# Performance work log

Hardware: AMD Instinct MI355X
Metric: run time of the kernel (lower is better)

## Reference

```python
import jax, jax.numpy as jnp
import numpy as np

B, P, T = 64, 49, 20      # batch, num_pixels (7x7), caption length
V, E, D, A, ENC = 32000, 512, 512, 512, 2048


def setup_inputs() -> dict:
    key = jax.random.key(0)
    ks = jax.random.split(key, 20)
    s = 0.02
    return {
        "features": jax.random.normal(ks[0], (B, P, ENC), jnp.float32),
        "captions": jax.random.randint(ks[1], (B, T), 0, V, jnp.int64),
        "embed_table": jax.random.normal(ks[2], (V, E), jnp.float32) * s,
        "W_ih": jax.random.normal(ks[3], (4 * D, ENC + E), jnp.float32) * s,
        "b_ih": jnp.zeros((4 * D,), jnp.float32),
        "W_hh": jax.random.normal(ks[4], (4 * D, D), jnp.float32) * s,
        "b_hh": jnp.zeros((4 * D,), jnp.float32),
        "W_init_h": jax.random.normal(ks[5], (ENC, D), jnp.float32) * s,
        "b_init_h": jnp.zeros((D,), jnp.float32),
        "W_init_c": jax.random.normal(ks[6], (ENC, D), jnp.float32) * s,
        "b_init_c": jnp.zeros((D,), jnp.float32),
        "W_enc_att": jax.random.normal(ks[7], (ENC, A), jnp.float32) * s,
        "b_enc_att": jnp.zeros((A,), jnp.float32),
        "W_dec_att": jax.random.normal(ks[8], (D, A), jnp.float32) * s,
        "b_dec_att": jnp.zeros((A,), jnp.float32),
        "w_A": jax.random.normal(ks[9], (A,), jnp.float32) * s,
        "b_A": jnp.zeros((), jnp.float32),
        "W_out": jax.random.normal(ks[10], (D, V), jnp.float32) * s,
        "b_out": jnp.zeros((V,), jnp.float32),
    }


def reference(features, captions, embed_table, W_ih, b_ih, W_hh, b_hh,
              W_init_h, b_init_h, W_init_c, b_init_c,
              W_enc_att, b_enc_att, W_dec_att, b_dec_att, w_A, b_A,
              W_out, b_out):
    # Dropout is treated as identity (eval mode) for a deterministic baseline.
    bsz, seq_len = captions.shape
    emb = embed_table[captions]                              # [B,T,E]
    mean_f = features.mean(axis=1)                           # [B,ENC]
    h0 = mean_f @ W_init_h + b_init_h                        # [B,D]
    c0 = mean_f @ W_init_c + b_init_c                        # [B,D]
    enc_states = features @ W_enc_att + b_enc_att            # [B,P,A] (precomputed, loop-invariant)

    def step(carry, x_t):
        h, c = carry
        dec = h @ W_dec_att + b_dec_att                      # [B,A]
        comb = jnp.tanh(enc_states + dec[:, None, :])        # [B,P,A]
        scores = comb @ w_A + b_A                            # [B,P]
        alpha = jax.nn.softmax(scores, axis=1)
        ctx = jnp.einsum('bpe,bp->be', features, alpha)      # [B,ENC]
        x = jnp.concatenate([ctx, x_t], axis=1)              # [B,ENC+E]
        gates = x @ W_ih.T + b_ih + h @ W_hh.T + b_hh        # [B,4D]
        i, f, g, o = jnp.split(gates, 4, axis=1)
        i, f, o = jax.nn.sigmoid(i), jax.nn.sigmoid(f), jax.nn.sigmoid(o)
        g = jnp.tanh(g)
        c2 = f * c + i * g
        h2 = o * jnp.tanh(c2)
        logits = h2 @ W_out + b_out                          # [B,V]
        return (h2, c2), logits

    xs = jnp.swapaxes(emb[:, :seq_len - 1], 0, 1)            # [T-1,B,E]
    _, preds = jax.lax.scan(step, (h0, c0), xs)              # [T-1,B,V]
    preds = jnp.swapaxes(preds, 0, 1)                        # [B,T-1,V]
    vocab = W_out.shape[1]
    last = jnp.zeros((bsz, 1, vocab), preds.dtype)           # t = T-1 never written
    return jnp.concatenate([preds, last], axis=1)            # [B,T,V]
```

## Files before the change

kernel.cpp:

```cpp
#include <hip/hip_runtime.h>

constexpr int B_   = 64;
constexpr int P_   = 49;
constexpr int T_   = 20;
constexpr int V_   = 32000;
constexpr int E_   = 512;
constexpr int D_   = 512;
constexpr int A_   = 512;
constexpr int ENC_ = 2048;
constexpr int NT_  = T_ - 1;
constexpr int KX_  = ENC_ + E_ + D_;
constexpr int KSPL = 8;
constexpr int GCH  = (KX_ / 64) / KSPL;
constexpr int KS4  = 4;

#define DI __device__ __forceinline__

using u16 = unsigned short;
typedef short   bf16x8 __attribute__((ext_vector_type(8)));
typedef float   f32x4  __attribute__((ext_vector_type(4)));
typedef u16     u16x4  __attribute__((ext_vector_type(4)));

DI float sigm(float x) { return 1.0f / (1.0f + __expf(-x)); }
DI float tanhx(float x) {
  x = fminf(15.0f, fmaxf(-15.0f, x));
  float e = __expf(2.0f * x);
  return (e - 1.0f) / (e + 1.0f);
}
DI u16 f2bf(float x) {
  union { float f; unsigned u; } v{x};
  unsigned r = v.u + 0x7FFF + ((v.u >> 16) & 1);
  return (u16)(r >> 16);
}
DI float bf2f(u16 x) {
  union { unsigned u; float f; } v;
  v.u = ((unsigned)x) << 16;
  return v.f;
}
DI f32x4 mfma16(bf16x8 a, bf16x8 b, f32x4 c) {
  return __builtin_amdgcn_mfma_f32_16x16x32_bf16(a, b, c, 0, 0, 0);
}

constexpr int PRO1_BLOCKS = 32256;

DI void dev_tr_cvt(const float* in, u16* outp, int R, int C, int bx, int by,
                   float (*tbuf)[33]) {
  int tx = threadIdx.x & 31, ty = threadIdx.x >> 5;
  int c0 = bx * 32, r0 = by * 32;
#pragma unroll
  for (int i = 0; i < 4; i++)
    tbuf[ty + 8 * i][tx] = in[(size_t)(r0 + ty + 8 * i) * C + c0 + tx];
  __syncthreads();
#pragma unroll
  for (int i = 0; i < 4; i++)
    outp[(size_t)(c0 + ty + 8 * i) * R + r0 + tx] = f2bf(tbuf[tx][ty + 8 * i]);
}

__global__ __launch_bounds__(256) void k_pro1(
    const float* __restrict__ feat, const float* __restrict__ Winh,
    const float* __restrict__ Winc, const float* __restrict__ Wenc,
    const float* __restrict__ Wdec, const float* __restrict__ Wout,
    const float* __restrict__ Wih, const float* __restrict__ Whh,
    u16* __restrict__ mfb, u16* __restrict__ featb, u16* __restrict__ WiT,
    u16* __restrict__ WeT, u16* __restrict__ WdT, u16* __restrict__ WoT,
    u16* __restrict__ Wg) {
  __shared__ float tbuf[32][33];
  int bid = blockIdx.x;
  if (bid < 6272) {
    int i = bid * 256 + threadIdx.x;
    float4 v = ((const float4*)feat)[i];
    u16x4 r = {f2bf(v.x), f2bf(v.y), f2bf(v.z), f2bf(v.w)};
    ((u16x4*)featb)[i] = r;
  } else if (bid < 6784) {
    int idx = (bid - 6272) * 256 + threadIdx.x;
    int b = idx >> 11, e = idx & (ENC_ - 1);
    const float* f = feat + (size_t)b * P_ * ENC_ + e;
    float s = 0.f;
#pragma unroll
    for (int p = 0; p < P_; p++) s += f[(size_t)p * ENC_];
    mfb[idx] = f2bf(s * (1.0f / P_));
  } else if (bid < 7808) {
    int l = bid - 6784;
    dev_tr_cvt(Winh, WiT, ENC_, D_, l & 15, l >> 4, tbuf);
  } else if (bid < 8832) {
    int l = bid - 7808;
    dev_tr_cvt(Winc, WiT + (size_t)D_ * ENC_, ENC_, D_, l & 15, l >> 4, tbuf);
  } else if (bid < 9856) {
    int l = bid - 8832;
    dev_tr_cvt(Wenc, WeT, ENC_, A_, l & 15, l >> 4, tbuf);
  } else if (bid < 10112) {
    int l = bid - 9856;
    dev_tr_cvt(Wdec, WdT, D_, A_, l & 15, l >> 4, tbuf);
  } else if (bid < 26112) {
    int l = bid - 10112;
    dev_tr_cvt(Wout, WoT, D_, V_, l % 1000, l / 1000, tbuf);
  } else {
    int i = (bid - 26112) * 256 + threadIdx.x;
    int j = i / 768, rem = i - j * 768;
    int k = rem * 4;
    const float* src = (k < ENC_ + E_) ? (Wih + (size_t)j * (ENC_ + E_) + k)
                                       : (Whh + (size_t)j * D_ + (k - ENC_ - E_));
    float4 v = *(const float4*)src;
    u16x4 r = {f2bf(v.x), f2bf(v.y), f2bf(v.z), f2bf(v.w)};
    ((u16x4*)Wg)[i] = r;
  }
}


__global__ __launch_bounds__(256) void k_pro2(const u16* __restrict__ mfb,
    const u16* __restrict__ WiT, const float* __restrict__ binh,
    const float* __restrict__ binc, u16* __restrict__ hbf,
    float* __restrict__ c, const u16* __restrict__ featb,
    const u16* __restrict__ WeT, const float* __restrict__ benc,
    float* __restrict__ encs) {
  int wid = threadIdx.x >> 6, lane = threadIdx.x & 63;
  int l16 = lane & 15, lk = lane >> 4;
  if (blockIdx.x < 16) {
    int n0 = blockIdx.x * 64 + wid * 16;
    const u16* bp = WiT + (size_t)(n0 + l16) * ENC_ + 8 * lk;
    const u16* ap = mfb + (size_t)l16 * ENC_ + 8 * lk;
    f32x4 acc[4] = {};
#pragma unroll 4
    for (int kc = 0; kc < ENC_; kc += 32) {
      bf16x8 b = *(const bf16x8*)(bp + kc);
#pragma unroll
      for (int mf = 0; mf < 4; mf++) {
        bf16x8 a = *(const bf16x8*)(ap + (size_t)mf * 16 * ENC_ + kc);
        acc[mf] = mfma16(a, b, acc[mf]);
      }
    }
    int n = n0 + l16;
#pragma unroll
    for (int mf = 0; mf < 4; mf++) {
      int m = mf * 16 + 4 * lk;
#pragma unroll
      for (int r = 0; r < 4; r++) {
        float v = acc[mf][r];
        if (n < D_) hbf[(size_t)(m + r) * D_ + n] = f2bf(v + binh[n]);
        else        c[(size_t)(m + r) * D_ + (n - D_)] = v + binc[n - D_];
      }
    }
  } else {
    int l = blockIdx.x - 16;
    int m0 = (l % 49) * 64, n0 = (l / 49) * 64 + wid * 16;
    const u16* ap = featb + (size_t)(m0 + l16) * ENC_ + 8 * lk;
    const u16* bp = WeT + (size_t)(n0 + l16) * ENC_ + 8 * lk;
    f32x4 acc[4] = {};
#pragma unroll 8
    for (int i = 0; i < ENC_ / 32; i++) {
      int kc = i * 32;
      bf16x8 b = *(const bf16x8*)(bp + kc);
#pragma unroll
      for (int mf = 0; mf < 4; mf++) {
        bf16x8 a = *(const bf16x8*)(ap + (size_t)mf * 16 * ENC_ + kc);
        acc[mf] = mfma16(a, b, acc[mf]);
      }
    }
    float bv = benc[n0 + l16];
#pragma unroll
    for (int mf = 0; mf < 4; mf++) {
      int m = m0 + mf * 16 + 4 * lk;
#pragma unroll
      for (int r = 0; r < 4; r++)
        encs[(size_t)(m + r) * A_ + n0 + l16] = acc[mf][r] + bv;
    }
  }
}


__global__ __launch_bounds__(512) void k_att5(const u16* __restrict__ featb,
    const float* __restrict__ encs, const u16* __restrict__ WdT,
    const float* __restrict__ bdec, const float* __restrict__ wA,
    const float* __restrict__ bA, const float* __restrict__ gp,
    const float* __restrict__ bih, const float* __restrict__ bhh,
    float* __restrict__ c, u16* __restrict__ hbf, u16* __restrict__ hallp,
    u16* __restrict__ ctxb, const int* __restrict__ cap,
    const float* __restrict__ tab, u16* __restrict__ embt, int t,
    int do_reduce, int do_att) {
  __shared__ u16 hsb[D_];
  __shared__ float ds[A_];
  __shared__ float sc[P_];
  __shared__ float inv_s;
  int b = blockIdx.x, tid = threadIdx.x;

  if (do_att) {
    int tok = cap[b * T_ + t];
    embt[(size_t)b * E_ + tid] = f2bf(tab[(size_t)tok * E_ + tid]);
  }

  if (do_reduce) {
    int d = tid;
    float g0 = 0, g1 = 0, g2 = 0, g3 = 0;
#pragma unroll
    for (int s = 0; s < KS4; s++) {
      const float* g = gp + (size_t)(s * B_ + b) * (4 * D_);
      g0 += g[d]; g1 += g[D_ + d]; g2 += g[2 * D_ + d]; g3 += g[3 * D_ + d];
    }
    g0 += bih[d] + bhh[d];
    g1 += bih[D_ + d] + bhh[D_ + d];
    g2 += bih[2 * D_ + d] + bhh[2 * D_ + d];
    g3 += bih[3 * D_ + d] + bhh[3 * D_ + d];
    float iv = sigm(g0), fv = sigm(g1), gv = tanhx(g2), ov = sigm(g3);
    float cv = fmaf(fv, c[b * D_ + d], iv * gv);
    float hv = ov * tanhx(cv);
    c[b * D_ + d] = cv;
    u16 hb = f2bf(hv);
    hsb[d] = hb;
    hbf[b * D_ + d] = hb;
    hallp[b * D_ + d] = hb;
  } else {
    hsb[tid] = hbf[b * D_ + tid];
  }
  __syncthreads();
  if (!do_att) return;

  {
    int w = tid >> 6, lane = tid & 63, l16 = lane & 15, lk = lane >> 4;
#pragma unroll
    for (int f = 0; f < 4; f++) {
      int n = w * 64 + f * 16 + l16;
      const u16* bp = WdT + (size_t)n * D_ + 8 * lk;
      f32x4 acc = {};
#pragma unroll
      for (int kc = 0; kc < D_; kc += 32) {
        bf16x8 av = *(const bf16x8*)(hsb + kc + 8 * lk);
        bf16x8 bv = *(const bf16x8*)(bp + kc);
        acc = mfma16(av, bv, acc);
      }
      if (lk == 0) ds[n] = acc[0] + bdec[n];
    }
  }
  __syncthreads();

  {
    int wv_ = tid >> 6, ln = tid & 63;
    float bA0 = bA[0];
    for (int p = wv_; p < P_; p += 8) {
      const float* ep = encs + (size_t)(b * P_ + p) * A_;
      float s = 0.f;
#pragma unroll
      for (int a = ln; a < A_; a += 64) s += tanhx(ep[a] + ds[a]) * wA[a];
#pragma unroll
      for (int off = 32; off; off >>= 1) s += __shfl_down(s, off);
      if (ln == 0) sc[p] = s + bA0;
    }
  }
  __syncthreads();
  if (tid == 0) {
    float mx = -1e30f;
    for (int p = 0; p < P_; p++) mx = fmaxf(mx, sc[p]);
    float sum = 0.f;
    for (int p = 0; p < P_; p++) { float ex = __expf(sc[p] - mx); sc[p] = ex; sum += ex; }
    inv_s = 1.0f / sum;
  }
  __syncthreads();
  {
    float inv = inv_s;
    int e = tid * 4;
    const u16* fp = featb + (size_t)b * P_ * ENC_ + e;
    float s0 = 0.f, s1 = 0.f, s2 = 0.f, s3 = 0.f;
#pragma unroll
    for (int p = 0; p < P_; p++) {
      u16x4 w = *(const u16x4*)(fp + (size_t)p * ENC_);
      float scp = sc[p];
      s0 = fmaf(bf2f(w.x), scp, s0);
      s1 = fmaf(bf2f(w.y), scp, s1);
      s2 = fmaf(bf2f(w.z), scp, s2);
      s3 = fmaf(bf2f(w.w), scp, s3);
    }
    u16x4 o = {f2bf(s0 * inv), f2bf(s1 * inv), f2bf(s2 * inv), f2bf(s3 * inv)};
    *(u16x4*)(ctxb + b * ENC_ + e) = o;
  }
}

__global__ __launch_bounds__(256) void k_gates4(const u16* __restrict__ ctxb,
    const u16* __restrict__ embt, const u16* __restrict__ hbf,
    const u16* __restrict__ Wg, float* __restrict__ gp) {
  int wid = threadIdx.x >> 6, lane = threadIdx.x & 63;
  int j0 = blockIdx.x * 64 + wid * 16;
  int sp = blockIdx.y;
  int l16 = lane & 15, lk = lane >> 4;
  const u16* bp = Wg + (size_t)(j0 + l16) * KX_ + 8 * lk;
  f32x4 acc[4] = {};
#pragma unroll
  for (int i = 0; i < KX_ / KS4 / 32; i++) {
    int kc = sp * (KX_ / KS4) + i * 32;
    int k = kc + 8 * lk;
    bf16x8 b = *(const bf16x8*)(bp + kc);
#pragma unroll
    for (int mf = 0; mf < 4; mf++) {
      int row = mf * 16 + l16;
      const u16* src;
      if (k < ENC_)            src = ctxb + (size_t)row * ENC_ + k;
      else if (k < ENC_ + E_)  src = embt + (size_t)row * E_ + (k - ENC_);
      else                     src = hbf + (size_t)row * D_ + (k - ENC_ - E_);
      bf16x8 a = *(const bf16x8*)src;
      acc[mf] = mfma16(a, b, acc[mf]);
    }
  }
#pragma unroll
  for (int mf = 0; mf < 4; mf++) {
    int m = mf * 16 + 4 * lk;
#pragma unroll
    for (int r = 0; r < 4; r++)
      gp[((size_t)sp * B_ + m + r) * (4 * D_) + j0 + l16] = acc[mf][r];
  }
}


__global__ __launch_bounds__(256) void k_logits_all4(const u16* __restrict__ hall,
    const u16* __restrict__ WoT, const float* __restrict__ bout,
    float* __restrict__ out) {
  __shared__ float tile[64 * 264];
  int L = blockIdx.x;
  int x8 = L & 7, r = L >> 3;
  int g = r / 24, s = r % 24;
  int nt = g * 8 + x8;
  if (nt >= 125) return;
  if (s == NT_) {
    int tr = threadIdx.x >> 2, tc = threadIdx.x & 3;
    f32x4 z = {0.f, 0.f, 0.f, 0.f};
    float* op = out + ((size_t)tr * T_ + NT_) * V_ + nt * 256;
#pragma unroll
    for (int j = 0; j < 16; j++)
      __builtin_nontemporal_store(z, (f32x4*)(op + (tc + j * 4) * 4));
    return;
  }
  if (s > NT_) return;
  int w = threadIdx.x >> 6, lane = threadIdx.x & 63;
  int l16 = lane & 15, lk = lane >> 4;
  const u16* ap0 = hall + (size_t)s * B_ * D_ + (size_t)l16 * D_ + 8 * lk;
  int ncol0 = nt * 256 + w * 64;
#pragma unroll 1
  for (int ch = 0; ch < 4; ch++) {
    int col = ncol0 + ch * 16 + l16;
    const u16* bp = WoT + (size_t)col * D_ + 8 * lk;
    f32x4 acc[4] = {};
#pragma unroll
    for (int kc = 0; kc < 16; kc++) {
      bf16x8 b = *(const bf16x8*)(bp + kc * 32);
#pragma unroll
      for (int mf = 0; mf < 4; mf++) {
        bf16x8 a = *(const bf16x8*)(ap0 + (size_t)mf * 16 * D_ + kc * 32);
        acc[mf] = mfma16(a, b, acc[mf]);
      }
    }
    float bv = bout[col];
#pragma unroll
    for (int mf = 0; mf < 4; mf++)
#pragma unroll
      for (int rr = 0; rr < 4; rr++)
        tile[(mf * 16 + 4 * lk + rr) * 264 + w * 64 + ch * 16 + l16] =
            acc[mf][rr] + bv;
  }
  __syncthreads();
  int tr = threadIdx.x >> 2, tc = threadIdx.x & 3;
  float* op = out + ((size_t)tr * T_ + s) * V_ + nt * 256;
  const float* lp = &tile[tr * 264];
#pragma unroll
  for (int j = 0; j < 16; j++) {
    int cc = (tc + j * 4) * 4;
    __builtin_nontemporal_store(*(const f32x4*)(lp + cc), (f32x4*)(op + cc));
  }
}


DI int swz(int row, int slot) { return row * 64 + ((slot ^ (row >> 2)) << 2); }

__global__ __launch_bounds__(256) void k_mean(const float* __restrict__ feat,
                                              float* __restrict__ mf) {
  int idx = blockIdx.x * 256 + threadIdx.x;
  int b = idx >> 11, e = idx & (ENC_ - 1);
  const float* f = feat + (size_t)b * P_ * ENC_ + e;
  float s = 0.f;
#pragma unroll
  for (int p = 0; p < P_; p++) s += f[(size_t)p * ENC_];
  mf[idx] = s * (1.0f / P_);
}

__global__ __launch_bounds__(256) void k_emb(const int* __restrict__ cap,
                                             const float* __restrict__ tab,
                                             float* __restrict__ emb) {
  int idx = blockIdx.x * 256 + threadIdx.x;
  int e  = idx & (E_ - 1);
  int bt = idx >> 9;
  int b = bt / NT_, t = bt - b * NT_;
  int tok = cap[b * T_ + t];
  emb[idx] = tab[(size_t)tok * E_ + e];
}

__global__ __launch_bounds__(256) void k_init(const float* __restrict__ mf,
    const float* __restrict__ Wh, const float* __restrict__ bh,
    const float* __restrict__ Wc, const float* __restrict__ bc,
    float* __restrict__ h, float* __restrict__ c) {
  __shared__ float ms[ENC_];
  int b = blockIdx.y;
  for (int i = threadIdx.x; i < ENC_; i += 256) ms[i] = mf[b * ENC_ + i];
  __syncthreads();
  int d = blockIdx.x * 256 + threadIdx.x;
  const float* W = blockIdx.z ? Wc : Wh;
  float s = (blockIdx.z ? bc : bh)[d];
#pragma unroll 8
  for (int e = 0; e < ENC_; e++) s = fmaf(ms[e], W[(size_t)e * D_ + d], s);
  (blockIdx.z ? c : h)[b * D_ + d] = s;
}

__global__ __launch_bounds__(256) void k_zero_last(float* __restrict__ out) {
  int i = blockIdx.x * 256 + threadIdx.x;
  int b = i / 8000, v4 = i - b * 8000;
  float4 z = {0.f, 0.f, 0.f, 0.f};
  *(float4*)(out + ((size_t)b * T_ + (T_ - 1)) * V_ + (size_t)v4 * 4) = z;
}

__global__ __launch_bounds__(256) void k_enc(const float* __restrict__ Ag,
    const float* __restrict__ Wg, const float* __restrict__ bias,
    float* __restrict__ Cg) {
  __shared__ float As[64 * 64], Ws[64 * 64];
  int m0 = blockIdx.x * 64, n0 = blockIdx.y * 64;
  int tid = threadIdx.x, tn = tid & 15, tm = tid >> 4;
  float acc[4][4] = {};
#pragma unroll 1
  for (int ch = 0; ch < ENC_ / 64; ch++) {
    int k0 = ch * 64;
    __syncthreads();
#pragma unroll
    for (int q = 0; q < 4; q++) {
      int idx = tid + q * 256;
      int row = idx >> 4, slot = idx & 15;
      *(float4*)&As[swz(row, slot)] =
          *(const float4*)(Ag + (size_t)(m0 + row) * ENC_ + k0 + slot * 4);
      *(float4*)&Ws[swz(row, slot)] =
          *(const float4*)(Wg + (size_t)(k0 + row) * A_ + n0 + slot * 4);
    }
    __syncthreads();
#pragma unroll
    for (int kk = 0; kk < 16; kk++) {
      float4 av[4], wv[4];
#pragma unroll
      for (int i = 0; i < 4; i++) av[i] = *(float4*)&As[swz(4 * tm + i, kk)];
#pragma unroll
      for (int u = 0; u < 4; u++) wv[u] = *(float4*)&Ws[swz(4 * kk + u, tn)];
      const float* wq = (const float*)wv;
#pragma unroll
      for (int i = 0; i < 4; i++) {
        const float* aq = (const float*)&av[i];
#pragma unroll
        for (int j = 0; j < 4; j++) {
          float s = acc[i][j];
#pragma unroll
          for (int u = 0; u < 4; u++) s = fmaf(aq[u], wq[u * 4 + j], s);
          acc[i][j] = s;
        }
      }
    }
  }
#pragma unroll
  for (int i = 0; i < 4; i++) {
    int m = m0 + 4 * tm + i, n = n0 + 4 * tn;
    float4 bv = *(const float4*)(bias + n);
    float4 o = {acc[i][0] + bv.x, acc[i][1] + bv.y, acc[i][2] + bv.z, acc[i][3] + bv.w};
    *(float4*)(Cg + (size_t)m * A_ + n) = o;
  }
}

__global__ __launch_bounds__(256) void k_logits(const float* __restrict__ h,
    const float* __restrict__ Wout, const float* __restrict__ bout,
    float* __restrict__ out, int t) {
  __shared__ float As[64 * 64], Ws[64 * 64];
  int n0 = blockIdx.x * 64;
  int tid = threadIdx.x, tn = tid & 15, tm = tid >> 4;
  float acc[4][4] = {};
#pragma unroll 1
  for (int ch = 0; ch < D_ / 64; ch++) {
    int k0 = ch * 64;
    __syncthreads();
#pragma unroll
    for (int q = 0; q < 4; q++) {
      int idx = tid + q * 256;
      int row = idx >> 4, slot = idx & 15;
      *(float4*)&As[swz(row, slot)] =
          *(const float4*)(h + (size_t)row * D_ + k0 + slot * 4);
      *(float4*)&Ws[swz(row, slot)] =
          *(const float4*)(Wout + (size_t)(k0 + row) * V_ + n0 + slot * 4);
    }
    __syncthreads();
#pragma unroll
    for (int kk = 0; kk < 16; kk++) {
      float4 av[4], wv[4];
#pragma unroll
      for (int i = 0; i < 4; i++) av[i] = *(float4*)&As[swz(4 * tm + i, kk)];
#pragma unroll
      for (int u = 0; u < 4; u++) wv[u] = *(float4*)&Ws[swz(4 * kk + u, tn)];
      const float* wq = (const float*)wv;
#pragma unroll
      for (int i = 0; i < 4; i++) {
        const float* aq = (const float*)&av[i];
#pragma unroll
        for (int j = 0; j < 4; j++) {
          float s = acc[i][j];
#pragma unroll
          for (int u = 0; u < 4; u++) s = fmaf(aq[u], wq[u * 4 + j], s);
          acc[i][j] = s;
        }
      }
    }
  }
#pragma unroll
  for (int i = 0; i < 4; i++) {
    int m = 4 * tm + i, n = n0 + 4 * tn;
    float4 bv = *(const float4*)(bout + n);
    float4 o = {acc[i][0] + bv.x, acc[i][1] + bv.y, acc[i][2] + bv.z, acc[i][3] + bv.w};
    *(float4*)(out + ((size_t)m * T_ + t) * V_ + n) = o;
  }
}

__global__ __launch_bounds__(256) void k_gates(const float* __restrict__ ctx,
    const float* __restrict__ emb, const float* __restrict__ h,
    const float* __restrict__ Wih, const float* __restrict__ Whh,
    float* __restrict__ gp, int t) {
  __shared__ float As[64 * 64], Ws[64 * 64];
  int n0 = blockIdx.x * 64;
  int sp = blockIdx.y;
  int tid = threadIdx.x, tn = tid & 15, tm = tid >> 4;
  float acc[4][4] = {};
#pragma unroll 1
  for (int ch = 0; ch < GCH; ch++) {
    int k0 = sp * (GCH * 64) + ch * 64;
    __syncthreads();
#pragma unroll
    for (int q = 0; q < 4; q++) {
      int idx = tid + q * 256;
      int row = idx >> 4, slot = idx & 15;
      int k = k0 + slot * 4;
      float4 xv;
      if (k < ENC_)            xv = *(const float4*)(ctx + (size_t)row * ENC_ + k);
      else if (k < ENC_ + E_)  xv = *(const float4*)(emb + ((size_t)row * NT_ + t) * E_ + (k - ENC_));
      else                     xv = *(const float4*)(h + (size_t)row * D_ + (k - ENC_ - E_));
      *(float4*)&As[swz(row, slot)] = xv;
      int j = n0 + row;
      float4 wv2;
      if (k < ENC_ + E_) wv2 = *(const float4*)(Wih + (size_t)j * (ENC_ + E_) + k);
      else               wv2 = *(const float4*)(Whh + (size_t)j * D_ + (k - ENC_ - E_));
      *(float4*)&Ws[swz(row, slot)] = wv2;
    }
    __syncthreads();
#pragma unroll
    for (int kk = 0; kk < 16; kk++) {
      float4 av[4], wv[4];
#pragma unroll
      for (int i = 0; i < 4; i++) av[i] = *(float4*)&As[swz(4 * tm + i, kk)];
#pragma unroll
      for (int j = 0; j < 4; j++) wv[j] = *(float4*)&Ws[swz(4 * tn + j, kk)];
#pragma unroll
      for (int i = 0; i < 4; i++) {
        const float* aq = (const float*)&av[i];
#pragma unroll
        for (int j = 0; j < 4; j++) {
          const float* wqj = (const float*)&wv[j];
          float s = acc[i][j];
#pragma unroll
          for (int u = 0; u < 4; u++) s = fmaf(aq[u], wqj[u], s);
          acc[i][j] = s;
        }
      }
    }
  }
#pragma unroll
  for (int i = 0; i < 4; i++) {
    int b = 4 * tm + i, j = n0 + 4 * tn;
    float4 o = {acc[i][0], acc[i][1], acc[i][2], acc[i][3]};
    *(float4*)(gp + ((size_t)(sp * B_ + b)) * (4 * D_) + j) = o;
  }
}

__global__ __launch_bounds__(512) void k_att(const float* __restrict__ feat,
    const float* __restrict__ encs, const float* __restrict__ Wdec,
    const float* __restrict__ bdec, const float* __restrict__ wA,
    const float* __restrict__ bA, const float* __restrict__ gp,
    const float* __restrict__ bih, const float* __restrict__ bhh,
    float* __restrict__ h, float* __restrict__ c, float* __restrict__ ctx,
    int do_reduce, int do_att) {
  __shared__ float hs[D_];
  __shared__ float ds[A_];
  __shared__ float sc[P_];
  __shared__ float inv_s;
  int b = blockIdx.x, tid = threadIdx.x;

  if (do_reduce) {
    int d = tid;
    float g0 = 0, g1 = 0, g2 = 0, g3 = 0;
#pragma unroll
    for (int s = 0; s < KSPL; s++) {
      const float* g = gp + (size_t)(s * B_ + b) * (4 * D_);
      g0 += g[d]; g1 += g[D_ + d]; g2 += g[2 * D_ + d]; g3 += g[3 * D_ + d];
    }
    g0 += bih[d] + bhh[d];
    g1 += bih[D_ + d] + bhh[D_ + d];
    g2 += bih[2 * D_ + d] + bhh[2 * D_ + d];
    g3 += bih[3 * D_ + d] + bhh[3 * D_ + d];
    float iv = sigm(g0), fv = sigm(g1), gv = tanhx(g2), ov = sigm(g3);
    float cv = fmaf(fv, c[b * D_ + d], iv * gv);
    float hv = ov * tanhx(cv);
    c[b * D_ + d] = cv;
    h[b * D_ + d] = hv;
    hs[d] = hv;
  } else {
    hs[tid] = h[b * D_ + tid];
  }
  __syncthreads();
  if (!do_att) return;

  {
    int a = tid;
    float s = bdec[a];
#pragma unroll 8
    for (int d = 0; d < D_; d++) s = fmaf(hs[d], Wdec[(size_t)d * A_ + a], s);
    ds[a] = s;
  }
  __syncthreads();

  int wv_ = tid >> 6, ln = tid & 63;
  float bA0 = bA[0];
  for (int p = wv_; p < P_; p += 8) {
    const float* ep = encs + (size_t)(b * P_ + p) * A_;
    float s = 0.f;
#pragma unroll
    for (int a = ln; a < A_; a += 64) s += tanhx(ep[a] + ds[a]) * wA[a];
#pragma unroll
    for (int off = 32; off; off >>= 1) s += __shfl_down(s, off);
    if (ln == 0) sc[p] = s + bA0;
  }
  __syncthreads();

  if (tid == 0) {
    float mx = -1e30f;
    for (int p = 0; p < P_; p++) mx = fmaxf(mx, sc[p]);
    float sum = 0.f;
    for (int p = 0; p < P_; p++) { float ex = __expf(sc[p] - mx); sc[p] = ex; sum += ex; }
    inv_s = 1.0f / sum;
  }
  __syncthreads();

  float inv = inv_s;
  for (int e = tid; e < ENC_; e += 512) {
    const float* fp = feat + (size_t)b * P_ * ENC_ + e;
    float s = 0.f;
#pragma unroll
    for (int p = 0; p < P_; p++) s = fmaf(fp[(size_t)p * ENC_], sc[p], s);
    ctx[b * ENC_ + e] = s * inv;
  }
}


extern "C" void kernel_launch(void* const* d_in, const int* in_sizes, int n_in,
                              void* d_out, int out_size, void* d_ws, size_t ws_size,
                              hipStream_t stream) {
  const float* features = (const float*)d_in[0];
  const int*   captions = (const int*)d_in[1];
  const float* table    = (const float*)d_in[2];
  const float* Wih  = (const float*)d_in[3];
  const float* bih  = (const float*)d_in[4];
  const float* Whh  = (const float*)d_in[5];
  const float* bhh  = (const float*)d_in[6];
  const float* Winh = (const float*)d_in[7];
  const float* binh = (const float*)d_in[8];
  const float* Winc = (const float*)d_in[9];
  const float* binc = (const float*)d_in[10];
  const float* Wenc = (const float*)d_in[11];
  const float* benc = (const float*)d_in[12];
  const float* Wdec = (const float*)d_in[13];
  const float* bdec = (const float*)d_in[14];
  const float* wA   = (const float*)d_in[15];
  const float* bA   = (const float*)d_in[16];
  const float* Wout = (const float*)d_in[17];
  const float* bout = (const float*)d_in[18];
  float* out = (float*)d_out;

  constexpr size_t F_ENC = (size_t)B_ * P_ * A_;
  constexpr size_t F_C   = (size_t)B_ * D_;
  constexpr size_t F_GP  = (size_t)KSPL * B_ * 4 * D_;
  constexpr size_t U_WOT = (size_t)V_ * D_;
  constexpr size_t U_WG  = (size_t)(4 * D_) * KX_;
  constexpr size_t U_HBF = (size_t)B_ * D_;
  constexpr size_t U_CTX = (size_t)B_ * ENC_;
  constexpr size_t U_FEAT = (size_t)B_ * P_ * ENC_;
  constexpr size_t U_WET = (size_t)A_ * ENC_;
  constexpr size_t U_WDT = (size_t)A_ * D_;
  constexpr size_t U_HALL = (size_t)NT_ * B_ * D_;
  static_assert((size_t)KS4 * B_ * 4 * D_ <= F_GP, "gp(KS4) fits");
  static_assert((size_t)B_ * E_ <= 2 * F_C, "embt fits in cbuf1");
  constexpr size_t NEED_BYTES =
      (F_ENC + 2 * F_C + F_GP) * 4 +
      (U_WOT + U_WG + U_HBF + U_CTX + U_FEAT + U_WET + U_HALL) * 2;
  constexpr size_t NEED2 = NEED_BYTES + U_WDT * 2;

  if (ws_size >= NEED2) {
    float* ws = (float*)d_ws;
    float* enc_states = ws;
    float* cbuf0  = enc_states + F_ENC;
    float* cbuf1  = cbuf0 + F_C;
    float* gparts = cbuf1 + F_C;
    u16* WoT   = (u16*)(gparts + F_GP);
    u16* Wg    = WoT + U_WOT;
    u16* hbf   = Wg + U_WG;
    u16* ctxb  = hbf + U_HBF;
    u16* featb = ctxb + U_CTX;
    u16* WeT   = featb + U_FEAT;
    u16* hall  = WeT + U_WET;
    u16* WdT   = hall + U_HALL;
    u16* WiT   = (u16*)gparts;
    u16* mfb   = ctxb;
    u16* embt  = (u16*)cbuf1;

    k_pro1<<<PRO1_BLOCKS, 256, 0, stream>>>(features, Winh, Winc, Wenc, Wdec,
                                            Wout, Wih, Whh, mfb, featb, WiT,
                                            WeT, WdT, WoT, Wg);
    k_pro2<<<408, 256, 0, stream>>>(mfb, WiT, binh, binc, hbf, cbuf0, featb,
                                    WeT, benc, enc_states);

    for (int t = 0; t < NT_; t++) {
      u16* hallp = (t > 0) ? (hall + (size_t)(t - 1) * B_ * D_) : hall;
      k_att5<<<64, 512, 0, stream>>>(featb, enc_states, WdT, bdec, wA, bA,
                                     gparts, bih, bhh, cbuf0, hbf, hallp, ctxb,
                                     captions, table, embt, t,
                                     t > 0 ? 1 : 0, 1);
      k_gates4<<<dim3(32, KS4), 256, 0, stream>>>(ctxb, embt, hbf, Wg, gparts);
    }
    k_att5<<<64, 512, 0, stream>>>(featb, enc_states, WdT, bdec, wA, bA,
                                   gparts, bih, bhh, cbuf0, hbf,
                                   hall + (size_t)(NT_ - 1) * B_ * D_, ctxb,
                                   captions, table, embt, 0, 1, 0);
    k_logits_all4<<<3072, 256, 0, stream>>>(hall, WoT, bout, out);
  } else {
    float* ws = (float*)d_ws;
    float* enc_states = ws;
    float* mean_f = enc_states + (size_t)B_ * P_ * A_;
    float* emb    = mean_f + (size_t)B_ * ENC_;
    float* h      = emb + (size_t)B_ * NT_ * E_;
    float* c      = h + (size_t)B_ * D_;
    float* ctx    = c + (size_t)B_ * D_;
    float* gparts = ctx + (size_t)B_ * ENC_;

    k_mean<<<512, 256, 0, stream>>>(features, mean_f);
    k_emb<<<2432, 256, 0, stream>>>(captions, table, emb);
    k_init<<<dim3(2, 64, 2), 256, 0, stream>>>(mean_f, Winh, binh, Winc, binc, h, c);
    k_enc<<<dim3(49, 8), 256, 0, stream>>>(features, Wenc, benc, enc_states);
    k_zero_last<<<2000, 256, 0, stream>>>(out);

    for (int t = 0; t < NT_; t++) {
      k_att<<<64, 512, 0, stream>>>(features, enc_states, Wdec, bdec, wA, bA,
                                    gparts, bih, bhh, h, c, ctx, t > 0 ? 1 : 0, 1);
      if (t > 0)
        k_logits<<<500, 256, 0, stream>>>(h, Wout, bout, out, t - 1);
      k_gates<<<dim3(32, KSPL), 256, 0, stream>>>(ctx, emb, h, Wih, Whh, gparts, t);
    }
    k_att<<<64, 512, 0, stream>>>(features, enc_states, Wdec, bdec, wA, bA,
                                  gparts, bih, bhh, h, c, ctx, 1, 0);
    k_logits<<<500, 256, 0, stream>>>(h, Wout, bout, out, NT_ - 1);
  }
}
```

Measured before the change: 1.349 ms.

## Split attention across two blocks per batch, widen gates K-split, add tiled W_out transpose

The W_out transpose moves out of the prologue into a dedicated kernel that reads coalesced float4 rows and writes 16-byte bf16 rows through a large shared tile. The per-step attention kernel now runs two blocks per batch row, each computing half of the context vector, with the LSTM cell state ping-ponged between two buffers so the duplicated block can redundantly recompute the cell update without racing. The gate GEMM's K-split goes from 4 to 8 for more parallelism, and h is written straight into the history buffer instead of a separate copy. The costs are duplicated attention-score work per batch, a larger partial-gate reduction, and heavy shared memory in the transpose kernel.

```diff
diff --git a/kernel.cpp b/kernel.cpp
--- a/kernel.cpp
+++ b/kernel.cpp
@@ -11,8 +11,6 @@
 constexpr int NT_  = T_ - 1;
 constexpr int KX_  = ENC_ + E_ + D_;
 constexpr int KSPL = 8;
-constexpr int GCH  = (KX_ / 64) / KSPL;
-constexpr int KS4  = 4;
 
 #define DI __device__ __forceinline__
 
@@ -20,6 +18,7 @@
 typedef short   bf16x8 __attribute__((ext_vector_type(8)));
 typedef float   f32x4  __attribute__((ext_vector_type(4)));
 typedef u16     u16x4  __attribute__((ext_vector_type(4)));
+typedef u16     u16x2  __attribute__((ext_vector_type(2)));
 
 DI float sigm(float x) { return 1.0f / (1.0f + __expf(-x)); }
 DI float tanhx(float x) {
@@ -41,7 +40,7 @@
   return __builtin_amdgcn_mfma_f32_16x16x32_bf16(a, b, c, 0, 0, 0);
 }
 
-constexpr int PRO1_BLOCKS = 32256;
+constexpr int PRO1_BLOCKS = 16256;
 
 DI void dev_tr_cvt(const float* in, u16* outp, int R, int C, int bx, int by,
                    float (*tbuf)[33]) {
@@ -56,14 +55,13 @@
     outp[(size_t)(c0 + ty + 8 * i) * R + r0 + tx] = f2bf(tbuf[tx][ty + 8 * i]);
 }
 
-__global__ __launch_bounds__(256) void k_pro1(
+__global__ __launch_bounds__(256) void k_pro1s(
     const float* __restrict__ feat, const float* __restrict__ Winh,
     const float* __restrict__ Winc, const float* __restrict__ Wenc,
-    const float* __restrict__ Wdec, const float* __restrict__ Wout,
-    const float* __restrict__ Wih, const float* __restrict__ Whh,
-    u16* __restrict__ mfb, u16* __restrict__ featb, u16* __restrict__ WiT,
-    u16* __restrict__ WeT, u16* __restrict__ WdT, u16* __restrict__ WoT,
-    u16* __restrict__ Wg) {
+    const float* __restrict__ Wdec, const float* __restrict__ Wih,
+    const float* __restrict__ Whh, u16* __restrict__ mfb,
+    u16* __restrict__ featb, u16* __restrict__ WiT, u16* __restrict__ WeT,
+    u16* __restrict__ WdT, u16* __restrict__ Wg) {
   __shared__ float tbuf[32][33];
   int bid = blockIdx.x;
   if (bid < 6272) {
@@ -91,11 +89,8 @@
   } else if (bid < 10112) {
     int l = bid - 9856;
     dev_tr_cvt(Wdec, WdT, D_, A_, l & 15, l >> 4, tbuf);
-  } else if (bid < 26112) {
-    int l = bid - 10112;
-    dev_tr_cvt(Wout, WoT, D_, V_, l % 1000, l / 1000, tbuf);
   } else {
-    int i = (bid - 26112) * 256 + threadIdx.x;
+    int i = (bid - 10112) * 256 + threadIdx.x;
     int j = i / 768, rem = i - j * 768;
     int k = rem * 4;
     const float* src = (k < ENC_ + E_) ? (Wih + (size_t)j * (ENC_ + E_) + k)
@@ -106,10 +101,32 @@
   }
 }
 
+__global__ __launch_bounds__(256) void k_trW(const float* __restrict__ in,
+                                             u16* __restrict__ outp) {
+  __shared__ u16 ld[128][264];
+  int v0 = blockIdx.x * 128, k0 = blockIdx.y * 256;
+  int vf = (threadIdx.x & 31) * 4, kk = threadIdx.x >> 5;
+#pragma unroll 4
+  for (int p = 0; p < 32; p++) {
+    int k = kk + p * 8;
+    float4 v = *(const float4*)(in + (size_t)(k0 + k) * V_ + v0 + vf);
+    ld[vf + 0][k] = f2bf(v.x);
+    ld[vf + 1][k] = f2bf(v.y);
+    ld[vf + 2][k] = f2bf(v.z);
+    ld[vf + 3][k] = f2bf(v.w);
+  }
+  __syncthreads();
+  int v = threadIdx.x >> 1, h = threadIdx.x & 1;
+  u16* op = outp + (size_t)(v0 + v) * D_ + k0 + h * 128;
+#pragma unroll
+  for (int i = 0; i < 16; i++)
+    *(bf16x8*)(op + i * 8) = *(const bf16x8*)(&ld[v][h * 128 + i * 8]);
+}
+
 
 __global__ __launch_bounds__(256) void k_pro2(const u16* __restrict__ mfb,
     const u16* __restrict__ WiT, const float* __restrict__ binh,
-    const float* __restrict__ binc, u16* __restrict__ hbf,
+    const float* __restrict__ binc, u16* __restrict__ hall0,
     float* __restrict__ c, const u16* __restrict__ featb,
     const u16* __restrict__ WeT, const float* __restrict__ benc,
     float* __restrict__ encs) {
@@ -136,7 +153,7 @@
 #pragma unroll
       for (int r = 0; r < 4; r++) {
         float v = acc[mf][r];
-        if (n < D_) hbf[(size_t)(m + r) * D_ + n] = f2bf(v + binh[n]);
+        if (n < D_) hall0[(size_t)(m + r) * D_ + n] = f2bf(v + binh[n]);
         else        c[(size_t)(m + r) * D_ + (n - D_)] = v + binc[n - D_];
       }
     }
@@ -168,22 +185,22 @@
 }
 
 
-__global__ __launch_bounds__(512) void k_att5(const u16* __restrict__ featb,
+__global__ __launch_bounds__(512) void k_att3(const u16* __restrict__ featb,
     const float* __restrict__ encs, const u16* __restrict__ WdT,
     const float* __restrict__ bdec, const float* __restrict__ wA,
     const float* __restrict__ bA, const float* __restrict__ gp,
     const float* __restrict__ bih, const float* __restrict__ bhh,
-    float* __restrict__ c, u16* __restrict__ hbf, u16* __restrict__ hallp,
-    u16* __restrict__ ctxb, const int* __restrict__ cap,
-    const float* __restrict__ tab, u16* __restrict__ embt, int t,
-    int do_reduce, int do_att) {
+    const float* __restrict__ c_in, float* __restrict__ c_out,
+    u16* __restrict__ hcur, u16* __restrict__ ctxb,
+    const int* __restrict__ cap, const float* __restrict__ tab,
+    u16* __restrict__ embt, int t, int do_reduce, int do_att) {
   __shared__ u16 hsb[D_];
   __shared__ float ds[A_];
   __shared__ float sc[P_];
   __shared__ float inv_s;
-  int b = blockIdx.x, tid = threadIdx.x;
-
-  if (do_att) {
+  int b = blockIdx.x, y = blockIdx.y, tid = threadIdx.x;
+
+  if (do_att && y == 0) {
     int tok = cap[b * T_ + t];
     embt[(size_t)b * E_ + tid] = f2bf(tab[(size_t)tok * E_ + tid]);
   }
@@ -192,7 +209,7 @@
     int d = tid;
     float g0 = 0, g1 = 0, g2 = 0, g3 = 0;
 #pragma unroll
-    for (int s = 0; s < KS4; s++) {
+    for (int s = 0; s < KSPL; s++) {
       const float* g = gp + (size_t)(s * B_ + b) * (4 * D_);
       g0 += g[d]; g1 += g[D_ + d]; g2 += g[2 * D_ + d]; g3 += g[3 * D_ + d];
     }
@@ -201,15 +218,16 @@
     g2 += bih[2 * D_ + d] + bhh[2 * D_ + d];
     g3 += bih[3 * D_ + d] + bhh[3 * D_ + d];
     float iv = sigm(g0), fv = sigm(g1), gv = tanhx(g2), ov = sigm(g3);
-    float cv = fmaf(fv, c[b * D_ + d], iv * gv);
+    float cv = fmaf(fv, c_in[b * D_ + d], iv * gv);
     float hv = ov * tanhx(cv);
-    c[b * D_ + d] = cv;
     u16 hb = f2bf(hv);
     hsb[d] = hb;
-    hbf[b * D_ + d] = hb;
-    hallp[b * D_ + d] = hb;
+    if (y == 0) {
+      c_out[b * D_ + d] = cv;
+      hcur[b * D_ + d] = hb;
+    }
   } else {
-    hsb[tid] = hbf[b * D_ + tid];
+    hsb[tid] = hcur[b * D_ + tid];
   }
   __syncthreads();
   if (!do_att) return;
@@ -254,27 +272,25 @@
     inv_s = 1.0f / sum;
   }
   __syncthreads();
+
   {
     float inv = inv_s;
-    int e = tid * 4;
+    int e = y * 1024 + tid * 2;
     const u16* fp = featb + (size_t)b * P_ * ENC_ + e;
-    float s0 = 0.f, s1 = 0.f, s2 = 0.f, s3 = 0.f;
+    float s0 = 0.f, s1 = 0.f;
 #pragma unroll
     for (int p = 0; p < P_; p++) {
-      u16x4 w = *(const u16x4*)(fp + (size_t)p * ENC_);
-      float scp = sc[p];
-      s0 = fmaf(bf2f(w.x), scp, s0);
-      s1 = fmaf(bf2f(w.y), scp, s1);
-      s2 = fmaf(bf2f(w.z), scp, s2);
-      s3 = fmaf(bf2f(w.w), scp, s3);
-    }
-    u16x4 o = {f2bf(s0 * inv), f2bf(s1 * inv), f2bf(s2 * inv), f2bf(s3 * inv)};
-    *(u16x4*)(ctxb + b * ENC_ + e) = o;
-  }
-}
-
-__global__ __launch_bounds__(256) void k_gates4(const u16* __restrict__ ctxb,
-    const u16* __restrict__ embt, const u16* __restrict__ hbf,
+      u16x2 w = *(const u16x2*)(fp + (size_t)p * ENC_);
+      s0 = fmaf(bf2f(w.x), sc[p], s0);
+      s1 = fmaf(bf2f(w.y), sc[p], s1);
+    }
+    u16x2 o = {f2bf(s0 * inv), f2bf(s1 * inv)};
+    *(u16x2*)(ctxb + b * ENC_ + e) = o;
+  }
+}
+
+__global__ __launch_bounds__(256) void k_gates_bf(const u16* __restrict__ ctxb,
+    const u16* __restrict__ embt, const u16* __restrict__ hcur,
     const u16* __restrict__ Wg, float* __restrict__ gp) {
   int wid = threadIdx.x >> 6, lane = threadIdx.x & 63;
   int j0 = blockIdx.x * 64 + wid * 16;
@@ -283,8 +299,8 @@
   const u16* bp = Wg + (size_t)(j0 + l16) * KX_ + 8 * lk;
   f32x4 acc[4] = {};
 #pragma unroll
-  for (int i = 0; i < KX_ / KS4 / 32; i++) {
-    int kc = sp * (KX_ / KS4) + i * 32;
+  for (int i = 0; i < KX_ / KSPL / 32; i++) {
+    int kc = sp * (KX_ / KSPL) + i * 32;
     int k = kc + 8 * lk;
     bf16x8 b = *(const bf16x8*)(bp + kc);
 #pragma unroll
@@ -293,7 +309,7 @@
       const u16* src;
       if (k < ENC_)            src = ctxb + (size_t)row * ENC_ + k;
       else if (k < ENC_ + E_)  src = embt + (size_t)row * E_ + (k - ENC_);
-      else                     src = hbf + (size_t)row * D_ + (k - ENC_ - E_);
+      else                     src = hcur + (size_t)row * D_ + (k - ENC_ - E_);
       bf16x8 a = *(const bf16x8*)src;
       acc[mf] = mfma16(a, b, acc[mf]);
     }
@@ -523,9 +539,10 @@
   int sp = blockIdx.y;
   int tid = threadIdx.x, tn = tid & 15, tm = tid >> 4;
   float acc[4][4] = {};
+  constexpr int GCH_ = (KX_ / 64) / KSPL;
 #pragma unroll 1
-  for (int ch = 0; ch < GCH; ch++) {
-    int k0 = sp * (GCH * 64) + ch * 64;
+  for (int ch = 0; ch < GCH_; ch++) {
+    int k0 = sp * (GCH_ * 64) + ch * 64;
     __syncthreads();
 #pragma unroll
     for (int q = 0; q < 4; q++) {
@@ -681,17 +698,15 @@
   constexpr size_t F_GP  = (size_t)KSPL * B_ * 4 * D_;
   constexpr size_t U_WOT = (size_t)V_ * D_;
   constexpr size_t U_WG  = (size_t)(4 * D_) * KX_;
-  constexpr size_t U_HBF = (size_t)B_ * D_;
+  constexpr size_t U_EMBT = (size_t)B_ * E_;
   constexpr size_t U_CTX = (size_t)B_ * ENC_;
   constexpr size_t U_FEAT = (size_t)B_ * P_ * ENC_;
   constexpr size_t U_WET = (size_t)A_ * ENC_;
   constexpr size_t U_WDT = (size_t)A_ * D_;
   constexpr size_t U_HALL = (size_t)NT_ * B_ * D_;
-  static_assert((size_t)KS4 * B_ * 4 * D_ <= F_GP, "gp(KS4) fits");
-  static_assert((size_t)B_ * E_ <= 2 * F_C, "embt fits in cbuf1");
   constexpr size_t NEED_BYTES =
       (F_ENC + 2 * F_C + F_GP) * 4 +
-      (U_WOT + U_WG + U_HBF + U_CTX + U_FEAT + U_WET + U_HALL) * 2;
+      (U_WOT + U_WG + U_EMBT + U_CTX + U_FEAT + U_WET + U_HALL) * 2;
   constexpr size_t NEED2 = NEED_BYTES + U_WDT * 2;
 
   if (ws_size >= NEED2) {
@@ -702,34 +717,40 @@
     float* gparts = cbuf1 + F_C;
     u16* WoT   = (u16*)(gparts + F_GP);
     u16* Wg    = WoT + U_WOT;
-    u16* hbf   = Wg + U_WG;
-    u16* ctxb  = hbf + U_HBF;
+    u16* embt  = Wg + U_WG;
+    u16* ctxb  = embt + U_EMBT;
     u16* featb = ctxb + U_CTX;
     u16* WeT   = featb + U_FEAT;
     u16* hall  = WeT + U_WET;
     u16* WdT   = hall + U_HALL;
     u16* WiT   = (u16*)gparts;
     u16* mfb   = ctxb;
-    u16* embt  = (u16*)cbuf1;
-
-    k_pro1<<<PRO1_BLOCKS, 256, 0, stream>>>(features, Winh, Winc, Wenc, Wdec,
-                                            Wout, Wih, Whh, mfb, featb, WiT,
-                                            WeT, WdT, WoT, Wg);
-    k_pro2<<<408, 256, 0, stream>>>(mfb, WiT, binh, binc, hbf, cbuf0, featb,
-                                    WeT, benc, enc_states);
+    float* cb[2] = {cbuf0, cbuf1};
+
+    k_pro1s<<<PRO1_BLOCKS, 256, 0, stream>>>(features, Winh, Winc, Wenc, Wdec,
+                                             Wih, Whh, mfb, featb, WiT, WeT,
+                                             WdT, Wg);
+    k_trW<<<dim3(V_ / 128, D_ / 256), 256, 0, stream>>>(Wout, WoT);
+    k_pro2<<<408, 256, 0, stream>>>(mfb, WiT, binh, binc, hall , cbuf0,
+                                    featb, WeT, benc, enc_states);
 
     for (int t = 0; t < NT_; t++) {
-      u16* hallp = (t > 0) ? (hall + (size_t)(t - 1) * B_ * D_) : hall;
-      k_att5<<<64, 512, 0, stream>>>(featb, enc_states, WdT, bdec, wA, bA,
-                                     gparts, bih, bhh, cbuf0, hbf, hallp, ctxb,
-                                     captions, table, embt, t,
-                                     t > 0 ? 1 : 0, 1);
-      k_gates4<<<dim3(32, KS4), 256, 0, stream>>>(ctxb, embt, hbf, Wg, gparts);
-    }
-    k_att5<<<64, 512, 0, stream>>>(featb, enc_states, WdT, bdec, wA, bA,
-                                   gparts, bih, bhh, cbuf0, hbf,
-                                   hall + (size_t)(NT_ - 1) * B_ * D_, ctxb,
-                                   captions, table, embt, 0, 1, 0);
+      u16* hcur = hall + (size_t)(t > 0 ? t - 1 : 0) * B_ * D_;
+      const float* cin = cb[(t > 0 ? (t - 1) : 0) & 1];
+      float* cout = cb[t & 1];
+      k_att3<<<dim3(64, 2), 512, 0, stream>>>(featb, enc_states, WdT, bdec, wA,
+                                              bA, gparts, bih, bhh, cin, cout,
+                                              hcur, ctxb, captions, table,
+                                              embt, t, t > 0 ? 1 : 0, 1);
+      k_gates_bf<<<dim3(32, KSPL), 256, 0, stream>>>(ctxb, embt, hcur, Wg,
+                                                     gparts);
+    }
+    k_att3<<<dim3(64, 1), 512, 0, stream>>>(featb, enc_states, WdT, bdec, wA,
+                                            bA, gparts, bih, bhh,
+                                            cb[(NT_ - 1) & 1], cb[NT_ & 1],
+                                            hall + (size_t)(NT_ - 1) * B_ * D_,
+                                            ctxb, captions, table, embt, 0,
+                                            1, 0);
     k_logits_all4<<<3072, 256, 0, stream>>>(hall, WoT, bout, out);
   } else {
     float* ws = (float*)d_ws;
```

Result: faster. 1.113 ms (-17.5%).
